# Kernel optimization log

Measured on AMD Instinct MI355X. Metric: run time of the kernel, lower is better.

The kernel has to match this reference:

```python
import jax, jax.numpy as jnp
import numpy as np

EPS = 1e-3
D_MODEL = 512
SEQ = 1024
BATCH = 4
N_LAYERS = 2
N_HEAD = 8
D_HEAD = 64
D_INNER = 1024


def _position_table(n_pos, d):
    # Faithful to PositionEncoding: sin applied to even cols; the cos line in
    # the source is a no-op (missing assignment), so odd cols stay raw.
    j = np.arange(d)
    pos = np.arange(n_pos)[:, None]
    pe = pos / np.power(10000.0, 2 * (j // 2) / d)
    pe[0] = 0.0
    pe[1:, 0::2] = np.sin(pe[1:, 0::2])
    return jnp.asarray(pe, dtype=jnp.float32)


def _layer_norm(z, a, b):
    # torch.std is unbiased (ddof=1); eps added to sigma, not variance
    mu = jnp.mean(z, axis=-1, keepdims=True)
    sigma = jnp.sqrt(jnp.sum((z - mu) ** 2, axis=-1, keepdims=True) / (z.shape[-1] - 1))
    return (z - mu) / (sigma + EPS) * a + b


def setup_inputs() -> dict:
    key = jax.random.key(0)
    ks = jax.random.split(key, 10)
    s = 0.02
    return {
        "x": jax.random.normal(ks[0], (BATCH, SEQ, D_MODEL), dtype=jnp.float32),
        "pos_enc": _position_table(SEQ, D_MODEL),
        "w_qs": jax.random.normal(ks[1], (N_LAYERS, N_HEAD, D_MODEL, D_HEAD), dtype=jnp.float32) * s,
        "w_ks": jax.random.normal(ks[2], (N_LAYERS, N_HEAD, D_MODEL, D_HEAD), dtype=jnp.float32) * s,
        "w_vs": jax.random.normal(ks[3], (N_LAYERS, N_HEAD, D_MODEL, D_HEAD), dtype=jnp.float32) * s,
        "ln1_a": jnp.ones((N_LAYERS, D_MODEL), dtype=jnp.float32),
        "ln1_b": jnp.zeros((N_LAYERS, D_MODEL), dtype=jnp.float32),
        "w1": jax.random.normal(ks[4], (N_LAYERS, D_INNER, D_MODEL), dtype=jnp.float32) * s,
        "b1": jax.random.normal(ks[5], (N_LAYERS, D_INNER), dtype=jnp.float32) * s,
        "w2": jax.random.normal(ks[6], (N_LAYERS, D_MODEL, D_INNER), dtype=jnp.float32) * s,
        "b2": jax.random.normal(ks[7], (N_LAYERS, D_MODEL), dtype=jnp.float32) * s,
        "ln2_a": jnp.ones((N_LAYERS, D_MODEL), dtype=jnp.float32),
        "ln2_b": jnp.zeros((N_LAYERS, D_MODEL), dtype=jnp.float32),
    }


def reference(x, pos_enc, w_qs, w_ks, w_vs, ln1_a, ln1_b, w1, b1, w2, b2, ln2_a, ln2_b):
    temper = jnp.sqrt(jnp.float32(D_MODEL))  # scale uses d_model, not d_k (as in source)
    x = x + pos_enc[None, :, :]
    for i in range(N_LAYERS):
        residual = x
        # per-head projections: [h, b, l, dk]
        q = jnp.einsum('bld,hdk->hblk', x, w_qs[i])
        k = jnp.einsum('bld,hdk->hblk', x, w_ks[i])
        v = jnp.einsum('bld,hdv->hblv', x, w_vs[i])
        attn = jax.nn.softmax(jnp.einsum('hbqk,hbmk->hbqm', q, k) / temper, axis=-1)
        out = jnp.einsum('hbqm,hbmv->hbqv', attn, v)
        # permute(1,2,0,3): concat heads along feature dim -> [b, l, h*dv]
        out = out.transpose(1, 2, 0, 3).reshape(BATCH, SEQ, N_HEAD * D_HEAD)
        x = _layer_norm(out + residual, ln1_a[i], ln1_b[i])
        # positionwise FFN (1x1 convs == linears)
        h = jax.nn.relu(jnp.einsum('bld,fd->blf', x, w1[i]) + b1[i])
        o = jnp.einsum('blf,df->bld', h, w2[i]) + b2[i]
        x = _layer_norm(o + x, ln2_a[i], ln2_b[i])
    return x
```

## Files before the change

### kernel.cpp

```cpp
#include <hip/hip_runtime.h>
#include <math.h>

#define D_MODEL 512
#define SEQ     1024
#define BATCH   4
#define N_LAYERS 2
#define N_HEAD  8
#define D_HEAD  64
#define D_INNER 1024
#define NTOK    (BATCH*SEQ)
#define LN_EPS  1e-3f

typedef float f32x4 __attribute__((ext_vector_type(4)));
typedef short bf16x8 __attribute__((ext_vector_type(8)));
typedef unsigned short ushort_t;
typedef unsigned int uint_t;
typedef unsigned long long ull_t;

__device__ inline ushort_t f2bf(float f) {
    uint_t u = __float_as_uint(f);
    u += 0x7FFFu + ((u >> 16) & 1u);
    return (ushort_t)(u >> 16);
}
__device__ inline float bf2f(ushort_t h) {
    return __uint_as_float((uint_t)h << 16);
}

__device__ __forceinline__ void gload16(const ushort_t* g, ushort_t* l) {
    __builtin_amdgcn_global_load_lds(
        (const __attribute__((address_space(1))) void*)g,
        (__attribute__((address_space(3))) void*)l, 16, 0, 0);
}

#define PREP_E0 (NTOK * D_MODEL)
#define PREP_E1 (1536 * 512)
#define PREP_EW (N_LAYERS * D_INNER * D_MODEL)
#define PREP_TOTAL (PREP_E0 + 2 * PREP_E1 + 2 * PREP_EW)

__global__ void prep_kernel(const float* __restrict__ x,
                            const float* __restrict__ pe,
                            const float* __restrict__ w_qs,
                            const float* __restrict__ w_ks,
                            const float* __restrict__ w_vs,
                            const float* __restrict__ w1,
                            const float* __restrict__ w2,
                            float* __restrict__ X,
                            ushort_t* __restrict__ Xraw,
                            ushort_t* __restrict__ Wqkv,
                            ushort_t* __restrict__ WqkvL,
                            ushort_t* __restrict__ W1b,
                            ushort_t* __restrict__ W2b) {
    int idx = blockIdx.x * 256 + threadIdx.x;
    if (idx < PREP_E0) {
        int l = (idx / D_MODEL) % SEQ;
        int d = idx % D_MODEL;
        float xv = x[idx];
        X[idx] = xv + pe[l * D_MODEL + d];
        Xraw[idx] = f2bf(xv);
        return;
    }
    idx -= PREP_E0;
    if (idx < 2 * PREP_E1) {
        int layer = idx / PREP_E1;
        int j = idx - layer * PREP_E1;
        int n = j >> 9, k = j & 511;
        int which = n >> 9, h = (n >> 6) & 7, d = n & 63;
        size_t wofs = (size_t)layer * N_HEAD * D_MODEL * D_HEAD;
        const float* W = (which == 0) ? w_qs + wofs
                       : (which == 1) ? w_ks + wofs : w_vs + wofs;
        float v = W[((size_t)h * D_MODEL + k) * D_HEAD + d];
        ushort_t hv = f2bf(v);
        Wqkv[(size_t)layer * PREP_E1 + j] = hv;
        if (layer == 0) WqkvL[j] = f2bf(v - bf2f(hv));
        return;
    }
    idx -= 2 * PREP_E1;
    if (idx < PREP_EW) { W1b[idx] = f2bf(w1[idx]); return; }
    idx -= PREP_EW;
    W2b[idx] = f2bf(w2[idx]);
}

__device__ inline void qkv_scatter(f32x4 a, int n, int m_base,
                                   const float* __restrict__ pew,
                                   ushort_t* Qhi, ushort_t* Qlo,
                                   ushort_t* Khi, ushort_t* Klo,
                                   ushort_t* Vt) {
    int which = n >> 9, hd = n & 511;
    int head = hd >> 6, d = hd & 63;
    int hb = head * BATCH + (m_base >> 10);
    int l  = m_base & 1023;
    if (pew) {
#pragma unroll
        for (int r = 0; r < 4; r++) a[r] += pew[(size_t)(l + r) * 1536 + n];
    }
    if (which == 2) {
        ushort4 pk = make_ushort4(f2bf(a[0]), f2bf(a[1]), f2bf(a[2]), f2bf(a[3]));
        *(ushort4*)(Vt + ((size_t)hb * D_HEAD + d) * SEQ + l) = pk;
    } else {
        ushort_t* H = (which == 0) ? Qhi : Khi;
        ushort_t* L = (which == 0) ? Qlo : Klo;
#pragma unroll
        for (int r = 0; r < 4; r++) {
            float v = a[r];
            ushort_t hv = f2bf(v);
            size_t off = ((size_t)hb * SEQ + l + r) * D_HEAD + d;
            H[off] = hv;
            L[off] = f2bf(v - bf2f(hv));
        }
    }
}

template<int MODE, int TM, int TN>
__global__ __launch_bounds__(256, (TM == 128 ? 3 : 4))
void gemm_kernel(const ushort_t* __restrict__ A, const ushort_t* __restrict__ Bt,
                 const float* __restrict__ bias, const float* __restrict__ pew,
                 float* __restrict__ outF, ushort_t* __restrict__ outB,
                 ushort_t* __restrict__ Qhi, ushort_t* __restrict__ Qlo,
                 ushort_t* __restrict__ Khi, ushort_t* __restrict__ Klo,
                 ushort_t* __restrict__ Vt,
                 int M, int N, int K) {
    constexpr int BK = 128;
    constexpr int WM = TM / 2, WN = TN / 2;
    constexpr int MT = WM / 16, NT = WN / 16;
    constexpr int WA = TM / 16;
    constexpr int WB = TN / 16;
    __shared__ ushort_t As[TM * BK];
    __shared__ ushort_t Bs[TN * BK];
    const int tid = threadIdx.x;
    const int m0 = blockIdx.y * TM, n0 = blockIdx.x * TN;
    const int w = tid >> 6, lane = tid & 63;
    const int wr = w >> 1, wc = w & 1;
    const int col = lane & 15, quad = lane >> 4;
    const int srow = lane >> 4;
    const int scc  = lane & 15;

    f32x4 acc[MT][NT] = {};

    for (int k0 = 0; k0 < K; k0 += BK) {
        __syncthreads();
#pragma unroll
        for (int q = 0; q < WA; q++) {
            int row = (w * WA + q) * 4 + srow;
            int sch = scc ^ (row & 7);
            gload16(A + (size_t)(m0 + row) * K + k0 + sch * 8,
                    &As[(w * WA + q) * 4 * BK]);
        }
#pragma unroll
        for (int q = 0; q < WB; q++) {
            int row = (w * WB + q) * 4 + srow;
            int sch = scc ^ (row & 7);
            gload16(Bt + (size_t)(n0 + row) * K + k0 + sch * 8,
                    &Bs[(w * WB + q) * 4 * BK]);
        }
        __syncthreads();
#pragma unroll
        for (int ks = 0; ks < BK; ks += 32) {
            const int cb = ks >> 3;
            const int sc_ = ((cb + quad) ^ (col & 7)) * 8;
            bf16x8 af[MT], bfr[NT];
#pragma unroll
            for (int t = 0; t < MT; t++)
                af[t] = *(const bf16x8*)(&As[(wr * WM + t * 16 + col) * BK + sc_]);
#pragma unroll
            for (int t = 0; t < NT; t++)
                bfr[t] = *(const bf16x8*)(&Bs[(wc * WN + t * 16 + col) * BK + sc_]);
#pragma unroll
            for (int mt = 0; mt < MT; mt++)
#pragma unroll
                for (int nt = 0; nt < NT; nt++)
                    acc[mt][nt] = __builtin_amdgcn_mfma_f32_16x16x32_bf16(
                        af[mt], bfr[nt], acc[mt][nt], 0, 0, 0);
        }
    }

#pragma unroll
    for (int mt = 0; mt < MT; mt++) {
#pragma unroll
        for (int nt = 0; nt < NT; nt++) {
            int n = n0 + wc * WN + nt * 16 + col;
            int m_base = m0 + wr * WM + mt * 16 + quad * 4;
            if (MODE == 0) {
                qkv_scatter(acc[mt][nt], n, m_base, pew, Qhi, Qlo, Khi, Klo, Vt);
            } else {
#pragma unroll
                for (int r = 0; r < 4; r++) {
                    int m = m_base + r;
                    float v = acc[mt][nt][r];
                    if (MODE == 1) {
                        float t = fmaxf(v + bias[n], 0.f);
                        outB[(size_t)m * N + n] = f2bf(t);
                    } else {
                        outF[(size_t)m * N + n] = v + bias[n];
                    }
                }
            }
        }
    }
}

__global__ __launch_bounds__(256, 4)
void gemm_hilo_kernel(const float* __restrict__ A,
                      const ushort_t* __restrict__ Bh,
                      const ushort_t* __restrict__ Bl,
                      float* __restrict__ outF, int M, int N, int K) {
    __shared__ ushort_t Ash[64][72];
    __shared__ ushort_t Asl[64][72];
    __shared__ ushort_t Bsh[64][72];
    __shared__ ushort_t Bsl[64][72];
    const int tid = threadIdx.x;
    const int m0 = blockIdx.y * 64, n0 = blockIdx.x * 64;
    const int w = tid >> 6, lane = tid & 63;
    const int wm = (w >> 1) * 32, wn = (w & 1) * 32;
    const int col = lane & 15, quad = lane >> 4;

    f32x4 acc[2][2] = {};

    for (int k0 = 0; k0 < K; k0 += 64) {
        __syncthreads();
#pragma unroll
        for (int p = 0; p < 4; p++) {
            int idx = p * 256 + tid;
            int row = idx >> 4, c4 = (idx & 15) * 4;
            float4 v = *(const float4*)(A + (size_t)(m0 + row) * K + k0 + c4);
            ushort_t h0 = f2bf(v.x), h1 = f2bf(v.y), h2 = f2bf(v.z), h3 = f2bf(v.w);
            *(ushort4*)(&Ash[row][c4]) = make_ushort4(h0, h1, h2, h3);
            *(ushort4*)(&Asl[row][c4]) = make_ushort4(
                f2bf(v.x - bf2f(h0)), f2bf(v.y - bf2f(h1)),
                f2bf(v.z - bf2f(h2)), f2bf(v.w - bf2f(h3)));
        }
#pragma unroll
        for (int p = 0; p < 2; p++) {
            int idx = p * 256 + tid;
            int row = idx >> 3, ch = (idx & 7) * 8;
            *(uint4*)(&Bsh[row][ch]) =
                *(const uint4*)(Bh + (size_t)(n0 + row) * K + k0 + ch);
            *(uint4*)(&Bsl[row][ch]) =
                *(const uint4*)(Bl + (size_t)(n0 + row) * K + k0 + ch);
        }
        __syncthreads();
#pragma unroll
        for (int ks = 0; ks < 64; ks += 32) {
            bf16x8 ah[2], al[2], bh[2], bl[2];
#pragma unroll
            for (int t = 0; t < 2; t++) {
                ah[t] = *(const bf16x8*)(&Ash[wm + t * 16 + col][ks + quad * 8]);
                al[t] = *(const bf16x8*)(&Asl[wm + t * 16 + col][ks + quad * 8]);
                bh[t] = *(const bf16x8*)(&Bsh[wn + t * 16 + col][ks + quad * 8]);
                bl[t] = *(const bf16x8*)(&Bsl[wn + t * 16 + col][ks + quad * 8]);
            }
#pragma unroll
            for (int mt = 0; mt < 2; mt++)
#pragma unroll
                for (int nt = 0; nt < 2; nt++) {
                    acc[mt][nt] = __builtin_amdgcn_mfma_f32_16x16x32_bf16(
                        ah[mt], bh[nt], acc[mt][nt], 0, 0, 0);
                    acc[mt][nt] = __builtin_amdgcn_mfma_f32_16x16x32_bf16(
                        ah[mt], bl[nt], acc[mt][nt], 0, 0, 0);
                    acc[mt][nt] = __builtin_amdgcn_mfma_f32_16x16x32_bf16(
                        al[mt], bh[nt], acc[mt][nt], 0, 0, 0);
                }
        }
    }

#pragma unroll
    for (int mt = 0; mt < 2; mt++)
#pragma unroll
        for (int nt = 0; nt < 2; nt++) {
            int n = n0 + wn + nt * 16 + col;
#pragma unroll
            for (int r = 0; r < 4; r++) {
                int m = m0 + wm + mt * 16 + quad * 4 + r;
                outF[(size_t)m * N + n] = acc[mt][nt][r];
            }
        }
}

template<bool HILO>
__global__ __launch_bounds__(256, 2)
void attention_kernel(const ushort_t* __restrict__ Qhi,
                      const ushort_t* __restrict__ Qlo,
                      const ushort_t* __restrict__ Khi,
                      const ushort_t* __restrict__ Klo,
                      const ushort_t* __restrict__ Vt,
                      float* __restrict__ P0,
                      float* __restrict__ P1,
                      float2* __restrict__ ML) {
    const int bid = blockIdx.x;
    const int split = bid >> 8;
    const int r8  = bid & 255;
    const int j   = r8 >> 3;
    const int hb  = (r8 & 7) * 4 + (j >> 3);
    const int qp2 = j & 7;
    const int h = hb >> 2, b = hb & 3;
    const int tid = threadIdx.x;
    const int w = tid >> 6, lane = tid & 63;
    const int col = lane & 15, quad = lane >> 4;
    const size_t kbase = (size_t)hb * SEQ * D_HEAD;
    const size_t vbase = (size_t)hb * D_HEAD * SEQ;

    __shared__ ushort_t Kh[2][64][72];
    __shared__ ushort_t Kl[HILO ? 2 : 1][64][72];
    __shared__ ushort_t Vs[2][64][72];
    __shared__ ushort_t Pl[4][2][16][72];

    const int srow0 = tid >> 3;
    const int srow1 = 32 + (tid >> 3);
    const int sch   = (tid & 7) * 8;

    const int qbase = qp2 * 128 + w * 32;
    bf16x8 qh[2][2], ql[2][2];
#pragma unroll
    for (int u = 0; u < 2; u++) {
        const ushort_t* qp = Qhi + kbase + (size_t)(qbase + u * 16 + col) * D_HEAD;
        qh[u][0] = *(const bf16x8*)(qp + quad * 8);
        qh[u][1] = *(const bf16x8*)(qp + 32 + quad * 8);
        if (HILO) {
            const ushort_t* lp = Qlo + kbase + (size_t)(qbase + u * 16 + col) * D_HEAD;
            ql[u][0] = *(const bf16x8*)(lp + quad * 8);
            ql[u][1] = *(const bf16x8*)(lp + 32 + quad * 8);
        }
    }

    f32x4 acco[2][4] = {};
    float mrun[2] = {-1e30f, -1e30f}, lrun[2] = {0.f, 0.f};
    const float inv_temper = 0.04419417382415922f;

    const int tbeg = split * (SEQ / 2);
    const int tend = tbeg + SEQ / 2;

    uint4 rK0, rK1, rL0, rL1, rV0, rV1;
    {
        const int t0 = tbeg;
        rK0 = *(const uint4*)(Khi + kbase + (size_t)(t0 + srow0) * D_HEAD + sch);
        rK1 = *(const uint4*)(Khi + kbase + (size_t)(t0 + srow1) * D_HEAD + sch);
        if (HILO) {
            rL0 = *(const uint4*)(Klo + kbase + (size_t)(t0 + srow0) * D_HEAD + sch);
            rL1 = *(const uint4*)(Klo + kbase + (size_t)(t0 + srow1) * D_HEAD + sch);
        }
        rV0 = *(const uint4*)(Vt + vbase + (size_t)srow0 * SEQ + t0 + sch);
        rV1 = *(const uint4*)(Vt + vbase + (size_t)srow1 * SEQ + t0 + sch);
        *(uint4*)(&Kh[0][srow0][sch]) = rK0;
        *(uint4*)(&Kh[0][srow1][sch]) = rK1;
        if (HILO) {
            *(uint4*)(&Kl[0][srow0][sch]) = rL0;
            *(uint4*)(&Kl[0][srow1][sch]) = rL1;
        }
        *(uint4*)(&Vs[0][srow0][sch]) = rV0;
        *(uint4*)(&Vs[0][srow1][sch]) = rV1;
    }
    __syncthreads();
    if (tbeg + 64 < tend) {
        const int tn = tbeg + 64;
        rK0 = *(const uint4*)(Khi + kbase + (size_t)(tn + srow0) * D_HEAD + sch);
        rK1 = *(const uint4*)(Khi + kbase + (size_t)(tn + srow1) * D_HEAD + sch);
        if (HILO) {
            rL0 = *(const uint4*)(Klo + kbase + (size_t)(tn + srow0) * D_HEAD + sch);
            rL1 = *(const uint4*)(Klo + kbase + (size_t)(tn + srow1) * D_HEAD + sch);
        }
        rV0 = *(const uint4*)(Vt + vbase + (size_t)srow0 * SEQ + tn + sch);
        rV1 = *(const uint4*)(Vt + vbase + (size_t)srow1 * SEQ + tn + sch);
    }

    int cur = 0;
    for (int t0 = tbeg; t0 < tend; t0 += 64) {
        float sc[2][4][4];
#pragma unroll
        for (int nt = 0; nt < 4; nt++) {
            bf16x8 kh0 = *(const bf16x8*)(&Kh[cur][nt * 16 + col][quad * 8]);
            bf16x8 kh1 = *(const bf16x8*)(&Kh[cur][nt * 16 + col][32 + quad * 8]);
            f32x4 s0 = {}, s1 = {};
            s0 = __builtin_amdgcn_mfma_f32_16x16x32_bf16(kh0, qh[0][0], s0, 0, 0, 0);
            s0 = __builtin_amdgcn_mfma_f32_16x16x32_bf16(kh1, qh[0][1], s0, 0, 0, 0);
            s1 = __builtin_amdgcn_mfma_f32_16x16x32_bf16(kh0, qh[1][0], s1, 0, 0, 0);
            s1 = __builtin_amdgcn_mfma_f32_16x16x32_bf16(kh1, qh[1][1], s1, 0, 0, 0);
            if (HILO) {
                bf16x8 kl0 = *(const bf16x8*)(&Kl[cur][nt * 16 + col][quad * 8]);
                bf16x8 kl1 = *(const bf16x8*)(&Kl[cur][nt * 16 + col][32 + quad * 8]);
                s0 = __builtin_amdgcn_mfma_f32_16x16x32_bf16(kl0, qh[0][0], s0, 0, 0, 0);
                s0 = __builtin_amdgcn_mfma_f32_16x16x32_bf16(kl1, qh[0][1], s0, 0, 0, 0);
                s0 = __builtin_amdgcn_mfma_f32_16x16x32_bf16(kh0, ql[0][0], s0, 0, 0, 0);
                s0 = __builtin_amdgcn_mfma_f32_16x16x32_bf16(kh1, ql[0][1], s0, 0, 0, 0);
                s1 = __builtin_amdgcn_mfma_f32_16x16x32_bf16(kl0, qh[1][0], s1, 0, 0, 0);
                s1 = __builtin_amdgcn_mfma_f32_16x16x32_bf16(kl1, qh[1][1], s1, 0, 0, 0);
                s1 = __builtin_amdgcn_mfma_f32_16x16x32_bf16(kh0, ql[1][0], s1, 0, 0, 0);
                s1 = __builtin_amdgcn_mfma_f32_16x16x32_bf16(kh1, ql[1][1], s1, 0, 0, 0);
            }
#pragma unroll
            for (int r = 0; r < 4; r++) {
                sc[0][nt][r] = s0[r] * inv_temper;
                sc[1][nt][r] = s1[r] * inv_temper;
            }
        }

#pragma unroll
        for (int u = 0; u < 2; u++) {
            float tmax = sc[u][0][0];
#pragma unroll
            for (int nt = 0; nt < 4; nt++)
#pragma unroll
                for (int r = 0; r < 4; r++) tmax = fmaxf(tmax, sc[u][nt][r]);
            tmax = fmaxf(tmax, __shfl_xor(tmax, 16, 64));
            tmax = fmaxf(tmax, __shfl_xor(tmax, 32, 64));

            float mn = fmaxf(mrun[u], tmax);
            float alpha = __expf(mrun[u] - mn);
            mrun[u] = mn;
            float tsum = 0.f;
#pragma unroll
            for (int nt = 0; nt < 4; nt++) {
                float p0 = __expf(sc[u][nt][0] - mn);
                float p1 = __expf(sc[u][nt][1] - mn);
                float p2 = __expf(sc[u][nt][2] - mn);
                float p3 = __expf(sc[u][nt][3] - mn);
                tsum += (p0 + p1) + (p2 + p3);
                ull_t pk = (ull_t)f2bf(p0) | ((ull_t)f2bf(p1) << 16)
                         | ((ull_t)f2bf(p2) << 32) | ((ull_t)f2bf(p3) << 48);
                *(ull_t*)(&Pl[w][u][col][nt * 16 + quad * 4]) = pk;
            }
            tsum += __shfl_xor(tsum, 16, 64);
            tsum += __shfl_xor(tsum, 32, 64);
            lrun[u] = lrun[u] * alpha + tsum;
#pragma unroll
            for (int nt = 0; nt < 4; nt++)
#pragma unroll
                for (int r = 0; r < 4; r++) acco[u][nt][r] *= alpha;
        }

        __threadfence_block();

        union { ulong2 uu; bf16x8 v; } pa[2][2];
#pragma unroll
        for (int u = 0; u < 2; u++) {
            pa[u][0].uu = *(const ulong2*)(&Pl[w][u][col][quad * 8]);
            pa[u][1].uu = *(const ulong2*)(&Pl[w][u][col][32 + quad * 8]);
        }
#pragma unroll
        for (int nt = 0; nt < 4; nt++) {
            bf16x8 bv0 = *(const bf16x8*)(&Vs[cur][nt * 16 + col][quad * 8]);
            bf16x8 bv1 = *(const bf16x8*)(&Vs[cur][nt * 16 + col][32 + quad * 8]);
            acco[0][nt] = __builtin_amdgcn_mfma_f32_16x16x32_bf16(bv0, pa[0][0].v, acco[0][nt], 0, 0, 0);
            acco[0][nt] = __builtin_amdgcn_mfma_f32_16x16x32_bf16(bv1, pa[0][1].v, acco[0][nt], 0, 0, 0);
            acco[1][nt] = __builtin_amdgcn_mfma_f32_16x16x32_bf16(bv0, pa[1][0].v, acco[1][nt], 0, 0, 0);
            acco[1][nt] = __builtin_amdgcn_mfma_f32_16x16x32_bf16(bv1, pa[1][1].v, acco[1][nt], 0, 0, 0);
        }

        if (t0 + 64 < tend) {
            *(uint4*)(&Kh[cur ^ 1][srow0][sch]) = rK0;
            *(uint4*)(&Kh[cur ^ 1][srow1][sch]) = rK1;
            if (HILO) {
                *(uint4*)(&Kl[cur ^ 1][srow0][sch]) = rL0;
                *(uint4*)(&Kl[cur ^ 1][srow1][sch]) = rL1;
            }
            *(uint4*)(&Vs[cur ^ 1][srow0][sch]) = rV0;
            *(uint4*)(&Vs[cur ^ 1][srow1][sch]) = rV1;
            if (t0 + 128 < tend) {
                const int tn = t0 + 128;
                rK0 = *(const uint4*)(Khi + kbase + (size_t)(tn + srow0) * D_HEAD + sch);
                rK1 = *(const uint4*)(Khi + kbase + (size_t)(tn + srow1) * D_HEAD + sch);
                if (HILO) {
                    rL0 = *(const uint4*)(Klo + kbase + (size_t)(tn + srow0) * D_HEAD + sch);
                    rL1 = *(const uint4*)(Klo + kbase + (size_t)(tn + srow1) * D_HEAD + sch);
                }
                rV0 = *(const uint4*)(Vt + vbase + (size_t)srow0 * SEQ + tn + sch);
                rV1 = *(const uint4*)(Vt + vbase + (size_t)srow1 * SEQ + tn + sch);
            }
        }
        __syncthreads();
        cur ^= 1;
    }

    float* dst = split ? P1 : P0;
#pragma unroll
    for (int u = 0; u < 2; u++) {
        const int qrow = qbase + u * 16 + col;
#pragma unroll
        for (int nt = 0; nt < 4; nt++)
            *(f32x4*)(&dst[((size_t)b * SEQ + qrow) * D_MODEL + h * D_HEAD
                           + nt * 16 + quad * 4]) = acco[u][nt];
        if (quad == 0)
            ML[((size_t)split * 32 + hb) * SEQ + qrow] = make_float2(mrun[u], lrun[u]);
    }
}

__device__ __forceinline__ float wave_sum_64(float v) {
#pragma unroll
    for (int off = 32; off > 0; off >>= 1) v += __shfl_xor(v, off, 64);
    return v;
}

__global__ void add_norm_kernel(const float* __restrict__ A,
                                const float* __restrict__ R,
                                const float* __restrict__ ga,
                                const float* __restrict__ gb,
                                float* __restrict__ Out,
                                ushort_t* __restrict__ OutBf) {
    int tok = blockIdx.x * 4 + (threadIdx.x >> 6);
    int lane = threadIdx.x & 63;
    size_t base = (size_t)tok * D_MODEL + lane * 8;
    f32x4 a0 = *(const f32x4*)(A + base);
    f32x4 a1 = *(const f32x4*)(A + base + 4);
    f32x4 r0 = *(const f32x4*)(R + base);
    f32x4 r1 = *(const f32x4*)(R + base + 4);
    f32x4 z0, z1;
#pragma unroll
    for (int t = 0; t < 4; t++) { z0[t] = a0[t] + r0[t]; z1[t] = a1[t] + r1[t]; }
    float s = (z0[0] + z0[1] + z0[2] + z0[3]) + (z1[0] + z1[1] + z1[2] + z1[3]);
    s = wave_sum_64(s);
    float mu = s * (1.f / (float)D_MODEL);
    float ss = 0.f;
#pragma unroll
    for (int t = 0; t < 4; t++) {
        float d0 = z0[t] - mu, d1 = z1[t] - mu;
        ss += d0 * d0 + d1 * d1;
    }
    ss = wave_sum_64(ss);
    float sigma = sqrtf(ss * (1.f / (float)(D_MODEL - 1)));
    float inv = 1.f / (sigma + LN_EPS);
    f32x4 g0 = *(const f32x4*)(ga + lane * 8);
    f32x4 g1 = *(const f32x4*)(ga + lane * 8 + 4);
    f32x4 h0 = *(const f32x4*)(gb + lane * 8);
    f32x4 h1 = *(const f32x4*)(gb + lane * 8 + 4);
    f32x4 o0, o1;
    bf16x8 pk;
#pragma unroll
    for (int t = 0; t < 4; t++) {
        o0[t] = (z0[t] - mu) * inv * g0[t] + h0[t];
        o1[t] = (z1[t] - mu) * inv * g1[t] + h1[t];
        pk[t] = (short)f2bf(o0[t]);
        pk[t + 4] = (short)f2bf(o1[t]);
    }
    *(f32x4*)(Out + base) = o0;
    *(f32x4*)(Out + base + 4) = o1;
    *(bf16x8*)(OutBf + base) = pk;
}

__global__ void add_norm_combine_kernel(const float* __restrict__ Pa,
                                        const float* __restrict__ Pb,
                                        const float2* __restrict__ ML,
                                        const float* __restrict__ R,
                                        const float* __restrict__ ga,
                                        const float* __restrict__ gb,
                                        float* __restrict__ Out,
                                        ushort_t* __restrict__ OutBf) {
    int tok = blockIdx.x * 4 + (threadIdx.x >> 6);
    int lane = threadIdx.x & 63;
    int b = tok >> 10, l = tok & 1023;
    int hb0 = (lane >> 3) * 4 + b;
    float2 u0 = ML[(size_t)hb0 * SEQ + l];
    float2 u1 = ML[(size_t)(32 + hb0) * SEQ + l];
    float M = fmaxf(u0.x, u1.x);
    float e0 = __expf(u0.x - M), e1 = __expf(u1.x - M);
    float sinv = 1.f / (e0 * u0.y + e1 * u1.y);
    float sa = e0 * sinv, sb = e1 * sinv;
    size_t base = (size_t)tok * D_MODEL + lane * 8;
    f32x4 pa0 = *(const f32x4*)(Pa + base);
    f32x4 pa1 = *(const f32x4*)(Pa + base + 4);
    f32x4 pb0 = *(const f32x4*)(Pb + base);
    f32x4 pb1 = *(const f32x4*)(Pb + base + 4);
    f32x4 r0 = *(const f32x4*)(R + base);
    f32x4 r1 = *(const f32x4*)(R + base + 4);
    f32x4 z0, z1;
#pragma unroll
    for (int t = 0; t < 4; t++) {
        z0[t] = pa0[t] * sa + pb0[t] * sb + r0[t];
        z1[t] = pa1[t] * sa + pb1[t] * sb + r1[t];
    }
    float s = (z0[0] + z0[1] + z0[2] + z0[3]) + (z1[0] + z1[1] + z1[2] + z1[3]);
    s = wave_sum_64(s);
    float mu = s * (1.f / (float)D_MODEL);
    float ss = 0.f;
#pragma unroll
    for (int t = 0; t < 4; t++) {
        float d0 = z0[t] - mu, d1 = z1[t] - mu;
        ss += d0 * d0 + d1 * d1;
    }
    ss = wave_sum_64(ss);
    float sigma = sqrtf(ss * (1.f / (float)(D_MODEL - 1)));
    float inv = 1.f / (sigma + LN_EPS);
    f32x4 g0 = *(const f32x4*)(ga + lane * 8);
    f32x4 g1 = *(const f32x4*)(ga + lane * 8 + 4);
    f32x4 h0 = *(const f32x4*)(gb + lane * 8);
    f32x4 h1 = *(const f32x4*)(gb + lane * 8 + 4);
    f32x4 o0, o1;
    bf16x8 pk;
#pragma unroll
    for (int t = 0; t < 4; t++) {
        o0[t] = (z0[t] - mu) * inv * g0[t] + h0[t];
        o1[t] = (z1[t] - mu) * inv * g1[t] + h1[t];
        pk[t] = (short)f2bf(o0[t]);
        pk[t + 4] = (short)f2bf(o1[t]);
    }
    *(f32x4*)(Out + base) = o0;
    *(f32x4*)(Out + base + 4) = o1;
    *(bf16x8*)(OutBf + base) = pk;
}

extern "C" void kernel_launch(void* const* d_in, const int* in_sizes, int n_in,
                              void* d_out, int out_size, void* d_ws, size_t ws_size,
                              hipStream_t stream) {
    const float* x     = (const float*)d_in[0];
    const float* pe    = (const float*)d_in[1];
    const float* w_qs  = (const float*)d_in[2];
    const float* w_ks  = (const float*)d_in[3];
    const float* w_vs  = (const float*)d_in[4];
    const float* ln1_a = (const float*)d_in[5];
    const float* ln1_b = (const float*)d_in[6];
    const float* w1    = (const float*)d_in[7];
    const float* b1    = (const float*)d_in[8];
    const float* w2    = (const float*)d_in[9];
    const float* b2    = (const float*)d_in[10];
    const float* ln2_a = (const float*)d_in[11];
    const float* ln2_b = (const float*)d_in[12];
    float* out = (float*)d_out;

    const size_t NXD = (size_t)NTOK * D_MODEL;
    char* p = (char*)d_ws;
    float*    X    = (float*)p;     p += NXD * 4;
    float*    Ob   = (float*)p;     p += NXD * 4;
    ushort_t* Xbf  = (ushort_t*)p;  p += NXD * 2;
    ushort_t* Xraw = (ushort_t*)p;  p += NXD * 2;
    ushort_t* Qhi  = (ushort_t*)p;  p += NXD * 2;
    ushort_t* Qlo  = (ushort_t*)p;  p += NXD * 2;
    ushort_t* Khi  = (ushort_t*)p;  p += NXD * 2;
    ushort_t* Klo  = (ushort_t*)p;  p += NXD * 2;
    ushort_t* Vt   = (ushort_t*)p;  p += NXD * 2;
    ushort_t* Wqkv = (ushort_t*)p;  p += (size_t)N_LAYERS * 1536 * 512 * 2;
    ushort_t* WqkvL= (ushort_t*)p;  p += (size_t)1536 * 512 * 2;
    ushort_t* W1b  = (ushort_t*)p;  p += (size_t)N_LAYERS * D_INNER * D_MODEL * 2;
    ushort_t* W2b  = (ushort_t*)p;  p += (size_t)N_LAYERS * D_MODEL * D_INNER * 2;
    float2*   ML   = (float2*)p;
    ushort_t* Hbf  = Qhi;
    float*    PEW  = Ob;

    prep_kernel<<<(PREP_TOTAL + 255) / 256, 256, 0, stream>>>(
        x, pe, w_qs, w_ks, w_vs, w1, w2, X, Xraw, Wqkv, WqkvL, W1b, W2b);

    for (int i = 0; i < N_LAYERS; i++) {
        if (i == 0) {
            gemm_hilo_kernel<<<dim3(1536 / 64, SEQ / 64), 256, 0, stream>>>(
                pe, Wqkv, WqkvL, PEW, SEQ, 1536, D_MODEL);
            gemm_kernel<0, 128, 64><<<dim3(1536 / 64, NTOK / 128), 256, 0, stream>>>(
                Xraw, Wqkv, nullptr, PEW, nullptr, nullptr,
                Qhi, Qlo, Khi, Klo, Vt, NTOK, 1536, D_MODEL);
            attention_kernel<true><<<512, 256, 0, stream>>>(
                Qhi, Qlo, Khi, Klo, Vt, Ob, out, ML);
        } else {
            gemm_kernel<0, 128, 64><<<dim3(1536 / 64, NTOK / 128), 256, 0, stream>>>(
                Xbf, Wqkv + (size_t)i * 1536 * 512, nullptr, nullptr, nullptr,
                nullptr, Qhi, Qlo, Khi, Klo, Vt, NTOK, 1536, D_MODEL);
            attention_kernel<false><<<512, 256, 0, stream>>>(
                Qhi, Qlo, Khi, Klo, Vt, Ob, out, ML);
        }

        add_norm_combine_kernel<<<NTOK / 4, 256, 0, stream>>>(
            Ob, out, ML, X, ln1_a + i * D_MODEL, ln1_b + i * D_MODEL, X, Xbf);

        gemm_kernel<1, 128, 64><<<dim3(D_INNER / 64, NTOK / 128), 256, 0, stream>>>(
            Xbf, W1b + (size_t)i * D_INNER * D_MODEL, b1 + (size_t)i * D_INNER,
            nullptr, nullptr, Hbf, nullptr, nullptr, nullptr, nullptr, nullptr,
            NTOK, D_INNER, D_MODEL);

        gemm_kernel<2, 64, 64><<<dim3(D_MODEL / 64, NTOK / 64), 256, 0, stream>>>(
            Hbf, W2b + (size_t)i * D_MODEL * D_INNER, b2 + (size_t)i * D_MODEL,
            nullptr, Ob, nullptr, nullptr, nullptr, nullptr, nullptr, nullptr,
            NTOK, D_MODEL, D_INNER);

        float* dst = (i == N_LAYERS - 1) ? out : X;
        add_norm_kernel<<<NTOK / 4, 256, 0, stream>>>(
            Ob, X, ln2_a + i * D_MODEL, ln2_b + i * D_MODEL, dst, Xbf);
    }
}
```

Measured before the change: 268.1 us.

## Split-K the FFN down-projection and add lazy softmax rescaling in attention

The second FFN GEMM now splits its K dimension across two z-blocks. One half writes with bias to Ob and the other writes raw partials to a new Ob2 buffer, and add_norm_kernel sums both partials with the residual. This doubles the block count of a small 512-wide GEMM to fill more CUs, at the cost of an extra fp32 buffer write and read. Separately, the attention online softmax only rescales the running max, sum and accumulators when any lane's new tile max exceeds the running max by more than 8. This skips most exp and multiply work, but lets probabilities reach up to e^8 in bf16.

```diff
diff --git a/kernel.cpp b/kernel.cpp
--- a/kernel.cpp
+++ b/kernel.cpp
@@ -114,7 +114,8 @@
 __global__ __launch_bounds__(256, (TM == 128 ? 3 : 4))
 void gemm_kernel(const ushort_t* __restrict__ A, const ushort_t* __restrict__ Bt,
                  const float* __restrict__ bias, const float* __restrict__ pew,
-                 float* __restrict__ outF, ushort_t* __restrict__ outB,
+                 float* __restrict__ outF, float* __restrict__ outF2,
+                 ushort_t* __restrict__ outB,
                  ushort_t* __restrict__ Qhi, ushort_t* __restrict__ Qlo,
                  ushort_t* __restrict__ Khi, ushort_t* __restrict__ Klo,
                  ushort_t* __restrict__ Vt,
@@ -134,9 +135,12 @@
     const int srow = lane >> 4;
     const int scc  = lane & 15;
 
+    const int kbeg = (MODE == 2) ? (int)blockIdx.z * (K >> 1) : 0;
+    const int kend = (MODE == 2) ? kbeg + (K >> 1) : K;
+
     f32x4 acc[MT][NT] = {};
 
-    for (int k0 = 0; k0 < K; k0 += BK) {
+    for (int k0 = kbeg; k0 < kend; k0 += BK) {
         __syncthreads();
 #pragma unroll
         for (int q = 0; q < WA; q++) {
@@ -190,7 +194,10 @@
                         float t = fmaxf(v + bias[n], 0.f);
                         outB[(size_t)m * N + n] = f2bf(t);
                     } else {
-                        outF[(size_t)m * N + n] = v + bias[n];
+                        if (blockIdx.z == 0)
+                            outF[(size_t)m * N + n] = v + bias[n];
+                        else
+                            outF2[(size_t)m * N + n] = v;
                     }
                 }
             }
@@ -402,9 +409,17 @@
             tmax = fmaxf(tmax, __shfl_xor(tmax, 16, 64));
             tmax = fmaxf(tmax, __shfl_xor(tmax, 32, 64));
 
-            float mn = fmaxf(mrun[u], tmax);
-            float alpha = __expf(mrun[u] - mn);
-            mrun[u] = mn;
+            if (!__all(tmax - mrun[u] <= 8.f)) {
+                float mn = fmaxf(mrun[u], tmax);
+                float alpha = __expf(mrun[u] - mn);
+                mrun[u] = mn;
+                lrun[u] *= alpha;
+#pragma unroll
+                for (int nt = 0; nt < 4; nt++)
+#pragma unroll
+                    for (int r = 0; r < 4; r++) acco[u][nt][r] *= alpha;
+            }
+            const float mn = mrun[u];
             float tsum = 0.f;
 #pragma unroll
             for (int nt = 0; nt < 4; nt++) {
@@ -419,11 +434,7 @@
             }
             tsum += __shfl_xor(tsum, 16, 64);
             tsum += __shfl_xor(tsum, 32, 64);
-            lrun[u] = lrun[u] * alpha + tsum;
-#pragma unroll
-            for (int nt = 0; nt < 4; nt++)
-#pragma unroll
-                for (int r = 0; r < 4; r++) acco[u][nt][r] *= alpha;
+            lrun[u] += tsum;
         }
 
         __threadfence_block();
@@ -489,6 +500,7 @@
 }
 
 __global__ void add_norm_kernel(const float* __restrict__ A,
+                                const float* __restrict__ A2,
                                 const float* __restrict__ R,
                                 const float* __restrict__ ga,
                                 const float* __restrict__ gb,
@@ -499,11 +511,16 @@
     size_t base = (size_t)tok * D_MODEL + lane * 8;
     f32x4 a0 = *(const f32x4*)(A + base);
     f32x4 a1 = *(const f32x4*)(A + base + 4);
+    f32x4 c0 = *(const f32x4*)(A2 + base);
+    f32x4 c1 = *(const f32x4*)(A2 + base + 4);
     f32x4 r0 = *(const f32x4*)(R + base);
     f32x4 r1 = *(const f32x4*)(R + base + 4);
     f32x4 z0, z1;
 #pragma unroll
-    for (int t = 0; t < 4; t++) { z0[t] = a0[t] + r0[t]; z1[t] = a1[t] + r1[t]; }
+    for (int t = 0; t < 4; t++) {
+        z0[t] = a0[t] + c0[t] + r0[t];
+        z1[t] = a1[t] + c1[t] + r1[t];
+    }
     float s = (z0[0] + z0[1] + z0[2] + z0[3]) + (z1[0] + z1[1] + z1[2] + z1[3]);
     s = wave_sum_64(s);
     float mu = s * (1.f / (float)D_MODEL);
@@ -628,7 +645,8 @@
     ushort_t* WqkvL= (ushort_t*)p;  p += (size_t)1536 * 512 * 2;
     ushort_t* W1b  = (ushort_t*)p;  p += (size_t)N_LAYERS * D_INNER * D_MODEL * 2;
     ushort_t* W2b  = (ushort_t*)p;  p += (size_t)N_LAYERS * D_MODEL * D_INNER * 2;
-    float2*   ML   = (float2*)p;
+    float2*   ML   = (float2*)p;    p += (size_t)2 * 32 * SEQ * sizeof(float2);
+    float*    Ob2  = (float*)p;
     ushort_t* Hbf  = Qhi;
     float*    PEW  = Ob;
 
@@ -640,14 +658,14 @@
             gemm_hilo_kernel<<<dim3(1536 / 64, SEQ / 64), 256, 0, stream>>>(
                 pe, Wqkv, WqkvL, PEW, SEQ, 1536, D_MODEL);
             gemm_kernel<0, 128, 64><<<dim3(1536 / 64, NTOK / 128), 256, 0, stream>>>(
-                Xraw, Wqkv, nullptr, PEW, nullptr, nullptr,
+                Xraw, Wqkv, nullptr, PEW, nullptr, nullptr, nullptr,
                 Qhi, Qlo, Khi, Klo, Vt, NTOK, 1536, D_MODEL);
             attention_kernel<true><<<512, 256, 0, stream>>>(
                 Qhi, Qlo, Khi, Klo, Vt, Ob, out, ML);
         } else {
             gemm_kernel<0, 128, 64><<<dim3(1536 / 64, NTOK / 128), 256, 0, stream>>>(
                 Xbf, Wqkv + (size_t)i * 1536 * 512, nullptr, nullptr, nullptr,
-                nullptr, Qhi, Qlo, Khi, Klo, Vt, NTOK, 1536, D_MODEL);
+                nullptr, nullptr, Qhi, Qlo, Khi, Klo, Vt, NTOK, 1536, D_MODEL);
             attention_kernel<false><<<512, 256, 0, stream>>>(
                 Qhi, Qlo, Khi, Klo, Vt, Ob, out, ML);
         }
@@ -657,16 +675,16 @@
 
         gemm_kernel<1, 128, 64><<<dim3(D_INNER / 64, NTOK / 128), 256, 0, stream>>>(
             Xbf, W1b + (size_t)i * D_INNER * D_MODEL, b1 + (size_t)i * D_INNER,
-            nullptr, nullptr, Hbf, nullptr, nullptr, nullptr, nullptr, nullptr,
-            NTOK, D_INNER, D_MODEL);
-
-        gemm_kernel<2, 64, 64><<<dim3(D_MODEL / 64, NTOK / 64), 256, 0, stream>>>(
+            nullptr, nullptr, nullptr, Hbf, nullptr, nullptr, nullptr, nullptr,
+            nullptr, NTOK, D_INNER, D_MODEL);
+
+        gemm_kernel<2, 64, 64><<<dim3(D_MODEL / 64, NTOK / 64, 2), 256, 0, stream>>>(
             Hbf, W2b + (size_t)i * D_MODEL * D_INNER, b2 + (size_t)i * D_MODEL,
-            nullptr, Ob, nullptr, nullptr, nullptr, nullptr, nullptr, nullptr,
-            NTOK, D_MODEL, D_INNER);
+            nullptr, Ob, Ob2, nullptr, nullptr, nullptr, nullptr, nullptr,
+            nullptr, NTOK, D_MODEL, D_INNER);
 
         float* dst = (i == N_LAYERS - 1) ? out : X;
         add_norm_kernel<<<NTOK / 4, 256, 0, stream>>>(
-            Ob, X, ln2_a + i * D_MODEL, ln2_b + i * D_MODEL, dst, Xbf);
-    }
-}
+            Ob, Ob2, X, ln2_a + i * D_MODEL, ln2_b + i * D_MODEL, dst, Xbf);
+    }
+}
```

Measured after the change: 271.6 us. No clear change (+1.3%).
